# Kernel optimization log

Measured on AMD Instinct MI355X. Metric: run time of the kernel, lower is better.

Reference implementation:

```python
import jax, jax.numpy as jnp
import numpy as np

B, S, T = 1024, 1024, 32
TAGS = ["O"] + [p + f"T{i}" for i in range(1, 16) for p in ("B-", "I-")] + ["B-T16"]
MASKED = -1.0e4


def _init_params(key):
    bound = float(np.sqrt(6.0 / T))
    k1, k2, k3 = jax.random.split(key, 3)
    start = np.array(jax.random.uniform(k1, (T,), minval=-bound, maxval=bound))
    trans = np.array(jax.random.uniform(k2, (T, T), minval=-bound, maxval=bound))
    end = np.array(jax.random.uniform(k3, (T,), minval=-bound, maxval=bound))
    # structural BIO masking, as in _initialize_parameters
    for i, src in enumerate(TAGS):
        if src.startswith("I-"):
            start[i] = MASKED
        for j, tgt in enumerate(TAGS):
            if (src.startswith("B-") or src.startswith("I-")) and tgt.startswith("I-") and src[2:] != tgt[2:]:
                trans[i, j] = MASKED
            elif src == "O" and tgt.startswith("I-"):
                trans[i, j] = MASKED
    return jnp.asarray(start, jnp.float32), jnp.asarray(trans, jnp.float32), jnp.asarray(end, jnp.float32)


def setup_inputs() -> dict:
    key = jax.random.key(0)
    k_em, k_tag, k_len, k_par = jax.random.split(key, 4)
    emissions = jax.random.normal(k_em, (B, S, T), dtype=jnp.float32)
    tags = jax.random.randint(k_tag, (B, S), 0, T, dtype=jnp.int64) if jax.config.jax_enable_x64 else jax.random.randint(k_tag, (B, S), 0, T).astype(jnp.int32)
    lengths = jax.random.randint(k_len, (B,), S // 4, S + 1)
    mask = jnp.arange(S)[None, :] < lengths[:, None]  # prefix mask, bool [B, S]
    start_transitions, transitions, end_transitions = _init_params(k_par)
    return {
        "emissions": emissions,
        "tags": tags,
        "mask": mask,
        "start_transitions": start_transitions,
        "transitions": transitions,
        "end_transitions": end_transitions,
    }


def reference(emissions, tags, mask, start_transitions, transitions, end_transitions):
    b, s, t = emissions.shape
    ar = jnp.arange(s)
    bidx = jnp.arange(b)
    head = jnp.min(jnp.where(mask, ar[None, :], s - 1), axis=1)  # [B]
    tail = jnp.max(ar[None, :] * mask, axis=1)                   # [B]
    nonempty = mask.sum(axis=1) != 0

    # condition[:, j-1] == (mask[:, j] and head != j), for j = 1..S-1
    cond = mask[:, 1:] & (head[:, None] != ar[None, 1:])  # [B, S-1]

    # ---- numerator (gold path score): additive, fully vectorized ----
    head_tags = tags[bidx, head]
    tail_tags = tags[bidx, tail]
    em_tag = jnp.take_along_axis(emissions, tags[:, :, None], axis=2)[:, :, 0]  # [B, S]
    trans_step = transitions[tags[:, :-1], tags[:, 1:]]                          # [B, S-1]
    numerator = (start_transitions[head_tags]
                 + em_tag[bidx, head]
                 + jnp.sum(jnp.where(cond, trans_step + em_tag[:, 1:], 0.0), axis=1)
                 + end_transitions[tail_tags])
    numerator = jnp.where(nonempty, numerator, 0.0)

    # ---- denominator (log partition): scan over time ----
    score0 = start_transitions[None, :] + emissions[bidx, head]  # [B, T]

    def step(score, xs):
        em_j, cond_j = xs  # [B, T], [B]
        nxt = jax.nn.logsumexp(score[:, :, None] + transitions[None, :, :] + em_j[:, None, :], axis=1)
        return jnp.where(cond_j[:, None], nxt, score), None

    em_seq = jnp.moveaxis(emissions[:, 1:, :], 1, 0)  # [S-1, B, T]
    cond_seq = jnp.moveaxis(cond, 1, 0)               # [S-1, B]
    score_final, _ = jax.lax.scan(step, score0, (em_seq, cond_seq))
    denominator = jax.nn.logsumexp(score_final + end_transitions[None, :], axis=1)
    denominator = jnp.where(nonempty, denominator, 0.0)

    # ---- token_mean reduction ----
    llh = denominator - numerator
    labels = mask.sum(axis=1).astype(emissions.dtype)
    eps = 1e-6
    return jnp.sum(llh / (labels + eps)) / (jnp.sum(labels != 0).astype(emissions.dtype) + eps)
```

## Files before the change

### kernel.cpp

```cpp
#include <hip/hip_runtime.h>
#include <cstdint>

static constexpr int S = 1024;
static constexpr int T = 32;
static constexpr float L2E  = 1.4426950408889634f;
static constexpr float LN2f = 0.6931471805599453f;

typedef __attribute__((ext_vector_type(8)))  short  short8;
typedef __attribute__((ext_vector_type(16))) float  float16;

union Frag { unsigned u[4]; short8 s; };

__global__ void crf_zero(float* ws) {
  ws[0] = 0.0f; ws[1] = 0.0f; ((unsigned*)ws)[2] = 0u;
}

__device__ __forceinline__ float bcast_lane(float v, int k) {
  return __uint_as_float((unsigned)__builtin_amdgcn_readlane((int)__float_as_uint(v), k));
}

__device__ __forceinline__ unsigned pk2r(float lo, float hi) {
#if __has_builtin(__builtin_amdgcn_cvt_pk_bf16_f32)
  typedef __attribute__((ext_vector_type(2))) __bf16 bf162_t;
  union { bf162_t v; unsigned u; } r;
  r.v = __builtin_amdgcn_cvt_pk_bf16_f32(lo, hi);
  return r.u;
#else
  unsigned h_ = __float_as_uint(hi), l_ = __float_as_uint(lo);
  return ((h_ + 0x8000u) & 0xFFFF0000u) | ((l_ + 0x8000u) >> 16);
#endif
}

__device__ __forceinline__ unsigned pk2f(float lo, float hi) {
#if __has_builtin(__builtin_amdgcn_cvt_pk_bf16_f32)
  return pk2r(lo, hi);
#else
  return __builtin_amdgcn_perm(__float_as_uint(hi), __float_as_uint(lo), 0x07060302u);
#endif
}

__device__ __forceinline__ float lo16(unsigned w) { return __uint_as_float(w << 16); }
__device__ __forceinline__ float hi16(unsigned w) { return __uint_as_float(w & 0xFFFF0000u); }

__device__ __forceinline__ int sig(int k) {
  int g2 = (k >> 2) & 3;
  if (g2 == 1) g2 = 2; else if (g2 == 2) g2 = 1;
  return (k & ~12) | (g2 << 2);
}

__global__ __launch_bounds__(512, 4) void crf_main(
    const float* __restrict__ em, const int* __restrict__ tags,
    const int* __restrict__ mask, const float* __restrict__ startT,
    const float* __restrict__ trans, const float* __restrict__ endT,
    float* __restrict__ ws, float* __restrict__ out, int B)
{
  __shared__ __align__(16) unsigned s_g16[8 * 256];
  __shared__ __align__(16) unsigned s_mats[8 * 544];
  __shared__ float s_trans[1024];
  __shared__ short s_tags[1024];
  __shared__ unsigned long long s_mb[17];
  __shared__ int   s_head, s_tail, s_cnt, s_K[8];
  __shared__ float s_num[8];

  const int tid = threadIdx.x;
  const int l   = tid & 63;
  const int wv  = tid >> 6;
  const int b   = blockIdx.x;
  const int n   = l & 31;
  const int h   = l >> 5;

  const float* emb   = em   + (size_t)b * S * T;
  const int*   maskb = mask + (size_t)b * S;
  const int*   tagsb = tags + (size_t)b * S;

  for (int i = tid; i < 1024; i += 512) {
    s_tags[i]  = (short)tagsb[i];
    s_trans[i] = trans[i];
  }
  {
    unsigned long long b0 = __ballot(maskb[wv * 128 + l] != 0);
    unsigned long long b1 = __ballot(maskb[wv * 128 + 64 + l] != 0);
    if (l == 0) { s_mb[2 * wv] = b0; s_mb[2 * wv + 1] = b1; }
    if (tid == 0) s_mb[16] = 0ull;
  }

  Frag Alo, Ahi;
  #pragma unroll
  for (int p = 0; p < 4; ++p) {
    int k0 = 8 * h + 2 * p;
    Alo.u[p] = pk2r(exp2f(trans[sig(k0 + 0)      * T + n] * L2E),
                    exp2f(trans[sig(k0 + 1)      * T + n] * L2E));
    Ahi.u[p] = pk2r(exp2f(trans[sig(16 + k0 + 0) * T + n] * L2E),
                    exp2f(trans[sig(16 + k0 + 1) * T + n] * L2E));
  }
  __syncthreads();

  if (wv == 0) {
    int first = 0x7fffffff, last = -1, pc = 0;
    if (l < 16) {
      unsigned long long w = s_mb[l];
      if (w) {
        first = 64 * l + (int)__builtin_ctzll(w);
        last  = 64 * l + 63 - (int)__builtin_clzll(w);
        pc    = (int)__builtin_popcountll(w);
      }
    }
    #pragma unroll
    for (int d = 1; d < 64; d <<= 1) {
      first = min(first, __shfl_xor(first, d));
      last  = max(last,  __shfl_xor(last,  d));
      pc   += __shfl_xor(pc, d);
    }
    if (l == 0) { s_head = first; s_tail = last; s_cnt = pc; }
  }
  __syncthreads();
  const int cnt  = s_cnt;
  const int head = (cnt > 0) ? s_head : 0;
  const int tail = (cnt > 0) ? s_tail : 0;

  const int span = tail - head;
  const int Lc   = (span + 7) >> 3;
  const int c0   = head + 1 + wv * Lc;
  const int c1   = min(c0 + Lc, tail + 1);

  unsigned* sgw16 = s_g16 + wv * 256;
  Frag Blo, Bhi;
  #pragma unroll
  for (int p = 0; p < 4; ++p) {
    int k0 = 8 * h + 2 * p;
    Blo.u[p] = ((sig(k0) == n)          ? 0x3F80u : 0u) |
               ((sig(k0 + 1) == n)      ? 0x3F800000u : 0u);
    Bhi.u[p] = ((sig(16 + k0) == n)     ? 0x3F80u : 0u) |
               ((sig(16 + k0 + 1) == n) ? 0x3F800000u : 0u);
  }
  int   Kacc  = 0;
  float numer = 0.0f;

#define FOLD(JJ, RSC) do {                                                   \
    const uint2* gw = (const uint2*)(sgw16 + (JJ) * 16);                     \
    uint2 wa = gw[h], wb = gw[h + 2], wc = gw[h + 4], wd = gw[h + 6];        \
    float16 D = {0,0,0,0,0,0,0,0,0,0,0,0,0,0,0,0};                           \
    D = __builtin_amdgcn_mfma_f32_32x32x16_bf16(Alo.s, Blo.s, D, 0, 0, 0);   \
    D = __builtin_amdgcn_mfma_f32_32x32x16_bf16(Ahi.s, Bhi.s, D, 0, 0, 0);   \
    D[0]  *= lo16(wa.x); D[1]  *= hi16(wa.x);                                \
    D[2]  *= lo16(wa.y); D[3]  *= hi16(wa.y);                                \
    D[4]  *= lo16(wb.x); D[5]  *= hi16(wb.x);                                \
    D[6]  *= lo16(wb.y); D[7]  *= hi16(wb.y);                                \
    D[8]  *= lo16(wc.x); D[9]  *= hi16(wc.x);                                \
    D[10] *= lo16(wc.y); D[11] *= hi16(wc.y);                                \
    D[12] *= lo16(wd.x); D[13] *= hi16(wd.x);                                \
    D[14] *= lo16(wd.y); D[15] *= hi16(wd.y);                                \
    if (RSC) {                                                               \
      float mx = fmaxf(fmaxf(fmaxf(D[0], D[1]), fmaxf(D[2], D[3])),          \
                       fmaxf(fmaxf(D[4], D[5]), fmaxf(D[6], D[7])));         \
      mx = fmaxf(mx, fmaxf(fmaxf(fmaxf(D[8], D[9]),  fmaxf(D[10], D[11])),   \
                           fmaxf(fmaxf(D[12], D[13]), fmaxf(D[14], D[15]))));\
      mx = fmaxf(mx, __shfl_xor(mx, 1));  mx = fmaxf(mx, __shfl_xor(mx, 2)); \
      mx = fmaxf(mx, __shfl_xor(mx, 4));  mx = fmaxf(mx, __shfl_xor(mx, 8)); \
      mx = fmaxf(mx, __shfl_xor(mx, 16)); mx = fmaxf(mx, __shfl_xor(mx, 32));\
      int E = (int)((__float_as_uint(mx) >> 23) & 0xffu);                    \
      float sc = __uint_as_float((unsigned)(254 - E) << 23);                 \
      Kacc += E - 127;                                                       \
      _Pragma("unroll")                                                      \
      for (int q_ = 0; q_ < 16; ++q_) D[q_] *= sc;                           \
    }                                                                        \
    Blo.u[0] = pk2f(D[0],  D[1]);  Blo.u[1] = pk2f(D[2],  D[3]);             \
    Blo.u[2] = pk2f(D[4],  D[5]);  Blo.u[3] = pk2f(D[6],  D[7]);             \
    Bhi.u[0] = pk2f(D[8],  D[9]);  Bhi.u[1] = pk2f(D[10], D[11]);            \
    Bhi.u[2] = pk2f(D[12], D[13]); Bhi.u[3] = pk2f(D[14], D[15]);            \
  } while (0)

  for (int j0 = c0; j0 < c1; j0 += 16) {
    const int ns = min(16, c1 - j0);
    const int w = j0 >> 6, o = j0 & 63;
    unsigned long long bits = s_mb[w] >> o;
    if (o) bits |= s_mb[w + 1] << (64 - o);
    unsigned eff = (unsigned)(bits & 0xFFFFull) & (unsigned)((1u << ns) - 1u);

    {
      const int i0 = l, i1 = l + 64;
      const int r0 = min(j0 + (i0 >> 3), S - 1), q0 = i0 & 7;
      const int r1 = min(j0 + (i1 >> 3), S - 1), q1 = i1 & 7;
      float4 v0 = ((const float4*)(emb + (size_t)r0 * T))[q0];
      float4 v1 = ((const float4*)(emb + (size_t)r1 * T))[q1];
      uint2 p0 = make_uint2(pk2r(exp2f(v0.x * L2E), exp2f(v0.y * L2E)),
                            pk2r(exp2f(v0.z * L2E), exp2f(v0.w * L2E)));
      uint2 p1 = make_uint2(pk2r(exp2f(v1.x * L2E), exp2f(v1.y * L2E)),
                            pk2r(exp2f(v1.z * L2E), exp2f(v1.w * L2E)));
      ((uint2*)sgw16)[i0] = p0; ((uint2*)sgw16)[i1] = p1;
    }

    if (l < ns && ((eff >> l) & 1u)) {
      int j  = j0 + l;
      int tg = (int)s_tags[j], tp = (int)s_tags[j - 1];
      unsigned gword = sgw16[l * 16 + (tg >> 1)];
      float gval = (tg & 1) ? hi16(gword) : lo16(gword);
      numer += s_trans[tp * T + tg] + log2f(gval) * LN2f;
    }

    if (eff == 0xFFFFu) {
      #pragma unroll
      for (int jj = 0; jj < 16; ++jj) FOLD(jj, ((jj & 7) == 7));
    } else {
      for (int jj = 0; jj < ns; ++jj)
        if ((eff >> jj) & 1u) FOLD(jj, true);
    }
  }
#undef FOLD

  {
    unsigned* mw = s_mats + wv * 544;
    #pragma unroll
    for (int p = 0; p < 4; ++p) {
      mw[(sig(8 * h + 2 * p)      >> 1) * 34 + n] = Blo.u[p];
      mw[(sig(16 + 8 * h + 2 * p) >> 1) * 34 + n] = Bhi.u[p];
    }
  }
  #pragma unroll
  for (int d = 1; d < 64; d <<= 1) numer += __shfl_xor(numer, d);
  if (l == 0) { s_num[wv] = numer; s_K[wv] = Kacc; }
  __syncthreads();

  if (wv == 0) {
    const int t = n;
    const float em0 = emb[head * T + t];
    float sc0 = (startT[t] + em0) * L2E;
    float m0 = sc0;
    #pragma unroll
    for (int d = 1; d < 32; d <<= 1) m0 = fmaxf(m0, __shfl_xor(m0, d));
    float e = exp2f(sc0 - m0);
    float Mtot = m0;

    const unsigned sh = (t & 1) ? 0u : 16u;
    for (int c = 0; c < 8; ++c) {
      const unsigned* mw = s_mats + c * 544 + (t >> 1) * 34;
      float acc = 0.0f;
      #pragma unroll
      for (int q2 = 0; q2 < 16; ++q2) {
        uint2 w2 = *(const uint2*)(mw + 2 * q2);
        float vlo = __uint_as_float((w2.x << sh) & 0xFFFF0000u);
        float vhi = __uint_as_float((w2.y << sh) & 0xFFFF0000u);
        acc = fmaf(vlo, bcast_lane(e, 2 * q2), acc);
        acc = fmaf(vhi, bcast_lane(e, 2 * q2 + 1), acc);
      }
      e = acc;
      Mtot += (float)s_K[c];
      float mx = e;
      #pragma unroll
      for (int d = 1; d < 32; d <<= 1) mx = fmaxf(mx, __shfl_xor(mx, d));
      int E = (int)((__float_as_uint(mx) >> 23) & 0xffu);
      e *= __uint_as_float((unsigned)(254 - E) << 23);
      Mtot += (float)(E - 127);
    }

    float fv = e * exp2f(endT[t] * L2E);
    #pragma unroll
    for (int d = 1; d < 32; d <<= 1) fv += __shfl_xor(fv, d);
    float denom = (Mtot + log2f(fv)) * LN2f;

    if (l == 0) {
      if (cnt > 0) {
        float ntot = 0.0f;
        for (int wq = 0; wq < 8; ++wq) ntot += s_num[wq];
        int th = (int)s_tags[head], tt = (int)s_tags[tail];
        ntot += startT[th] + bcast_lane(em0, th) + endT[tt];
        atomicAdd(&ws[0], (denom - ntot) / ((float)cnt + 1e-6f));
        atomicAdd(&ws[1], 1.0f);
      }
      __threadfence();
      unsigned done = atomicAdd((unsigned*)ws + 2, 1u);
      if (done == (unsigned)(B - 1)) {
        __threadfence();
        out[0] = ws[0] / (ws[1] + 1e-6f);
      }
    }
  }
}

extern "C" void kernel_launch(void* const* d_in, const int* in_sizes, int n_in,
                              void* d_out, int out_size, void* d_ws, size_t ws_size,
                              hipStream_t stream) {
  const float* em     = (const float*)d_in[0];
  const int*   tags   = (const int*)d_in[1];
  const int*   mask   = (const int*)d_in[2];
  const float* startT = (const float*)d_in[3];
  const float* trans  = (const float*)d_in[4];
  const float* endT   = (const float*)d_in[5];
  float* out = (float*)d_out;
  float* ws  = (float*)d_ws;

  const int B = in_sizes[0] / (S * T);

  crf_zero<<<1, 1, 0, stream>>>(ws);
  crf_main<<<B, 512, 0, stream>>>(em, tags, mask, startT, trans, endT, ws, out, B);
}
```

Measured before the change: 281.6 us.

## Prefetch next emission chunk, keep gains in fp32 LDS, trim max reduction

Emission loads for the next 16-step chunk are issued before the current chunk's folds, so global latency overlaps the MFMA recurrence (software prefetch into registers). Exponentiated emissions are now stored in LDS as fp32 instead of packed bf16, which doubles LDS use per wave but removes the unpack work and the bf16 rounding of the emission weights. The per-fold max reduction swaps four cross-lane shuffles for a single xor-32 shuffle plus readfirstlane. bf16 packing now goes through inline asm, and launch bounds ask for 8 waves per EU, which may constrain registers. The shortened reduction only yields a true wave-wide max if the lane layout puts identical maxima within each half, so the rescale exponent could differ per lane if that assumption fails.

New measurement: 268.4 us. 4.7% less time.

```diff
diff --git a/kernel.cpp b/kernel.cpp
--- a/kernel.cpp
+++ b/kernel.cpp
@@ -19,28 +19,11 @@
   return __uint_as_float((unsigned)__builtin_amdgcn_readlane((int)__float_as_uint(v), k));
 }
 
-__device__ __forceinline__ unsigned pk2r(float lo, float hi) {
-#if __has_builtin(__builtin_amdgcn_cvt_pk_bf16_f32)
-  typedef __attribute__((ext_vector_type(2))) __bf16 bf162_t;
-  union { bf162_t v; unsigned u; } r;
-  r.v = __builtin_amdgcn_cvt_pk_bf16_f32(lo, hi);
-  return r.u;
-#else
-  unsigned h_ = __float_as_uint(hi), l_ = __float_as_uint(lo);
-  return ((h_ + 0x8000u) & 0xFFFF0000u) | ((l_ + 0x8000u) >> 16);
-#endif
-}
-
-__device__ __forceinline__ unsigned pk2f(float lo, float hi) {
-#if __has_builtin(__builtin_amdgcn_cvt_pk_bf16_f32)
-  return pk2r(lo, hi);
-#else
-  return __builtin_amdgcn_perm(__float_as_uint(hi), __float_as_uint(lo), 0x07060302u);
-#endif
-}
-
-__device__ __forceinline__ float lo16(unsigned w) { return __uint_as_float(w << 16); }
-__device__ __forceinline__ float hi16(unsigned w) { return __uint_as_float(w & 0xFFFF0000u); }
+__device__ __forceinline__ unsigned cvtpk(float lo, float hi) {
+  unsigned r;
+  asm("v_cvt_pk_bf16_f32 %0, %1, %2" : "=v"(r) : "v"(lo), "v"(hi));
+  return r;
+}
 
 __device__ __forceinline__ int sig(int k) {
   int g2 = (k >> 2) & 3;
@@ -48,13 +31,13 @@
   return (k & ~12) | (g2 << 2);
 }
 
-__global__ __launch_bounds__(512, 4) void crf_main(
+__global__ __launch_bounds__(512, 8) void crf_main(
     const float* __restrict__ em, const int* __restrict__ tags,
     const int* __restrict__ mask, const float* __restrict__ startT,
     const float* __restrict__ trans, const float* __restrict__ endT,
     float* __restrict__ ws, float* __restrict__ out, int B)
 {
-  __shared__ __align__(16) unsigned s_g16[8 * 256];
+  __shared__ __align__(16) float    s_g32[8 * 512];
   __shared__ __align__(16) unsigned s_mats[8 * 544];
   __shared__ float s_trans[1024];
   __shared__ short s_tags[1024];
@@ -88,10 +71,10 @@
   #pragma unroll
   for (int p = 0; p < 4; ++p) {
     int k0 = 8 * h + 2 * p;
-    Alo.u[p] = pk2r(exp2f(trans[sig(k0 + 0)      * T + n] * L2E),
-                    exp2f(trans[sig(k0 + 1)      * T + n] * L2E));
-    Ahi.u[p] = pk2r(exp2f(trans[sig(16 + k0 + 0) * T + n] * L2E),
-                    exp2f(trans[sig(16 + k0 + 1) * T + n] * L2E));
+    Alo.u[p] = cvtpk(exp2f(trans[sig(k0 + 0)      * T + n] * L2E),
+                     exp2f(trans[sig(k0 + 1)      * T + n] * L2E));
+    Ahi.u[p] = cvtpk(exp2f(trans[sig(16 + k0 + 0) * T + n] * L2E),
+                     exp2f(trans[sig(16 + k0 + 1) * T + n] * L2E));
   }
   __syncthreads();
 
@@ -123,7 +106,7 @@
   const int c0   = head + 1 + wv * Lc;
   const int c1   = min(c0 + Lc, tail + 1);
 
-  unsigned* sgw16 = s_g16 + wv * 256;
+  float* sgw32 = s_g32 + wv * 512;
   Frag Blo, Bhi;
   #pragma unroll
   for (int p = 0; p < 4; ++p) {
@@ -136,65 +119,70 @@
   int   Kacc  = 0;
   float numer = 0.0f;
 
+  float4 v0, v1;
+#define LOADEM(J0) do {                                                      \
+    const int r0_ = min((J0) + (l >> 3),     S - 1);                         \
+    const int r1_ = min((J0) + 8 + (l >> 3), S - 1);                         \
+    v0 = ((const float4*)(emb + (size_t)r0_ * T))[l & 7];                    \
+    v1 = ((const float4*)(emb + (size_t)r1_ * T))[l & 7];                    \
+  } while (0)
+
+#define STOREG() do {                                                        \
+    float4 g0_, g1_;                                                         \
+    g0_.x = exp2f(v0.x * L2E); g0_.y = exp2f(v0.y * L2E);                    \
+    g0_.z = exp2f(v0.z * L2E); g0_.w = exp2f(v0.w * L2E);                    \
+    g1_.x = exp2f(v1.x * L2E); g1_.y = exp2f(v1.y * L2E);                    \
+    g1_.z = exp2f(v1.z * L2E); g1_.w = exp2f(v1.w * L2E);                    \
+    ((float4*)sgw32)[l] = g0_; ((float4*)sgw32)[l + 64] = g1_;               \
+  } while (0)
+
 #define FOLD(JJ, RSC) do {                                                   \
-    const uint2* gw = (const uint2*)(sgw16 + (JJ) * 16);                     \
-    uint2 wa = gw[h], wb = gw[h + 2], wc = gw[h + 4], wd = gw[h + 6];        \
+    const float4* gw = (const float4*)(sgw32 + (JJ) * 32);                   \
+    float4 wa = gw[h], wb = gw[h + 2], wc = gw[h + 4], wd = gw[h + 6];       \
     float16 D = {0,0,0,0,0,0,0,0,0,0,0,0,0,0,0,0};                           \
     D = __builtin_amdgcn_mfma_f32_32x32x16_bf16(Alo.s, Blo.s, D, 0, 0, 0);   \
     D = __builtin_amdgcn_mfma_f32_32x32x16_bf16(Ahi.s, Bhi.s, D, 0, 0, 0);   \
-    D[0]  *= lo16(wa.x); D[1]  *= hi16(wa.x);                                \
-    D[2]  *= lo16(wa.y); D[3]  *= hi16(wa.y);                                \
-    D[4]  *= lo16(wb.x); D[5]  *= hi16(wb.x);                                \
-    D[6]  *= lo16(wb.y); D[7]  *= hi16(wb.y);                                \
-    D[8]  *= lo16(wc.x); D[9]  *= hi16(wc.x);                                \
-    D[10] *= lo16(wc.y); D[11] *= hi16(wc.y);                                \
-    D[12] *= lo16(wd.x); D[13] *= hi16(wd.x);                                \
-    D[14] *= lo16(wd.y); D[15] *= hi16(wd.y);                                \
+    D[0]  *= wa.x; D[1]  *= wa.y; D[2]  *= wa.z; D[3]  *= wa.w;              \
+    D[4]  *= wb.x; D[5]  *= wb.y; D[6]  *= wb.z; D[7]  *= wb.w;              \
+    D[8]  *= wc.x; D[9]  *= wc.y; D[10] *= wc.z; D[11] *= wc.w;              \
+    D[12] *= wd.x; D[13] *= wd.y; D[14] *= wd.z; D[15] *= wd.w;              \
     if (RSC) {                                                               \
       float mx = fmaxf(fmaxf(fmaxf(D[0], D[1]), fmaxf(D[2], D[3])),          \
                        fmaxf(fmaxf(D[4], D[5]), fmaxf(D[6], D[7])));         \
       mx = fmaxf(mx, fmaxf(fmaxf(fmaxf(D[8], D[9]),  fmaxf(D[10], D[11])),   \
                            fmaxf(fmaxf(D[12], D[13]), fmaxf(D[14], D[15]))));\
-      mx = fmaxf(mx, __shfl_xor(mx, 1));  mx = fmaxf(mx, __shfl_xor(mx, 2)); \
-      mx = fmaxf(mx, __shfl_xor(mx, 4));  mx = fmaxf(mx, __shfl_xor(mx, 8)); \
-      mx = fmaxf(mx, __shfl_xor(mx, 16)); mx = fmaxf(mx, __shfl_xor(mx, 32));\
+      mx = fmaxf(mx, __shfl_xor(mx, 32));             \
+      mx = __uint_as_float((unsigned)__builtin_amdgcn_readfirstlane(         \
+               (int)__float_as_uint(mx)));                                   \
       int E = (int)((__float_as_uint(mx) >> 23) & 0xffu);                    \
       float sc = __uint_as_float((unsigned)(254 - E) << 23);                 \
       Kacc += E - 127;                                                       \
       _Pragma("unroll")                                                      \
       for (int q_ = 0; q_ < 16; ++q_) D[q_] *= sc;                           \
     }                                                                        \
-    Blo.u[0] = pk2f(D[0],  D[1]);  Blo.u[1] = pk2f(D[2],  D[3]);             \
-    Blo.u[2] = pk2f(D[4],  D[5]);  Blo.u[3] = pk2f(D[6],  D[7]);             \
-    Bhi.u[0] = pk2f(D[8],  D[9]);  Bhi.u[1] = pk2f(D[10], D[11]);            \
-    Bhi.u[2] = pk2f(D[12], D[13]); Bhi.u[3] = pk2f(D[14], D[15]);            \
+    Blo.u[0] = cvtpk(D[0],  D[1]);  Blo.u[1] = cvtpk(D[2],  D[3]);           \
+    Blo.u[2] = cvtpk(D[4],  D[5]);  Blo.u[3] = cvtpk(D[6],  D[7]);           \
+    Bhi.u[0] = cvtpk(D[8],  D[9]);  Bhi.u[1] = cvtpk(D[10], D[11]);          \
+    Bhi.u[2] = cvtpk(D[12], D[13]); Bhi.u[3] = cvtpk(D[14], D[15]);          \
   } while (0)
+
+  if (c0 < c1) LOADEM(c0);
 
   for (int j0 = c0; j0 < c1; j0 += 16) {
     const int ns = min(16, c1 - j0);
+
+    STOREG();
+    if (j0 + 16 < c1) LOADEM(j0 + 16);
+
     const int w = j0 >> 6, o = j0 & 63;
     unsigned long long bits = s_mb[w] >> o;
     if (o) bits |= s_mb[w + 1] << (64 - o);
     unsigned eff = (unsigned)(bits & 0xFFFFull) & (unsigned)((1u << ns) - 1u);
 
-    {
-      const int i0 = l, i1 = l + 64;
-      const int r0 = min(j0 + (i0 >> 3), S - 1), q0 = i0 & 7;
-      const int r1 = min(j0 + (i1 >> 3), S - 1), q1 = i1 & 7;
-      float4 v0 = ((const float4*)(emb + (size_t)r0 * T))[q0];
-      float4 v1 = ((const float4*)(emb + (size_t)r1 * T))[q1];
-      uint2 p0 = make_uint2(pk2r(exp2f(v0.x * L2E), exp2f(v0.y * L2E)),
-                            pk2r(exp2f(v0.z * L2E), exp2f(v0.w * L2E)));
-      uint2 p1 = make_uint2(pk2r(exp2f(v1.x * L2E), exp2f(v1.y * L2E)),
-                            pk2r(exp2f(v1.z * L2E), exp2f(v1.w * L2E)));
-      ((uint2*)sgw16)[i0] = p0; ((uint2*)sgw16)[i1] = p1;
-    }
-
     if (l < ns && ((eff >> l) & 1u)) {
       int j  = j0 + l;
       int tg = (int)s_tags[j], tp = (int)s_tags[j - 1];
-      unsigned gword = sgw16[l * 16 + (tg >> 1)];
-      float gval = (tg & 1) ? hi16(gword) : lo16(gword);
+      float gval = sgw32[l * 32 + tg];
       numer += s_trans[tp * T + tg] + log2f(gval) * LN2f;
     }
 
@@ -207,6 +195,8 @@
     }
   }
 #undef FOLD
+#undef STOREG
+#undef LOADEM
 
   {
     unsigned* mw = s_mats + wv * 544;
```
